# Kernel optimization log

Hardware: AMD Instinct MI355X
Metric: run time of the kernel (lower is better)

The kernel has to match this reference:

```python
import jax, jax.numpy as jnp
import numpy as np

N_THRESH = 100  # thresholds = 0.00, 0.01, ..., 0.99


def setup_inputs() -> dict:
    key = jax.random.key(0)
    k1, k2 = jax.random.split(key)
    predicted_mask = jax.random.uniform(k1, (32, 1, 1024, 1024), dtype=jnp.float32)
    gt_mask = jax.random.randint(k2, (32, 1, 1024, 1024), 0, 2, dtype=jnp.int32)
    return {"predicted_mask": predicted_mask, "gt_mask": gt_mask}


def reference(predicted_mask, gt_mask):
    # Single-pass histogram formulation of: for each t_k in arange(0,1,0.01),
    # iou_k = |(pred > t_k) & gt| / |(pred > t_k) | gt|  (torchmetrics binary Jaccard,
    # strict '>' thresholding, safe-divide -> 0 when union is empty).
    thresholds = jnp.arange(0.0, 1.0, 0.01, dtype=jnp.float32)  # [100], sorted
    pred = jnp.squeeze(predicted_mask).ravel()                  # [N] probabilities in [0,1]
    gt = jnp.squeeze(gt_mask).ravel().astype(jnp.float32)       # [N] 0/1

    # cnt[i] = number of thresholds strictly below pred[i]; pixel i satisfies
    # (pred > t_k) exactly for k in [0, cnt[i]).
    cnt = jnp.searchsorted(thresholds, pred, side='left')       # [N] int in [0, 100]

    hist_pos = jax.ops.segment_sum(gt, cnt, num_segments=N_THRESH + 1)              # [101]
    hist_all = jax.ops.segment_sum(jnp.ones_like(gt), cnt, num_segments=N_THRESH + 1)

    # TP_k = #{pred > t_k and gt==1} = sum_{c > k} hist_pos[c]  (suffix sums via cumsum)
    tp = jnp.sum(hist_pos) - jnp.cumsum(hist_pos)[:N_THRESH]        # [100]
    pred_pos = jnp.sum(hist_all) - jnp.cumsum(hist_all)[:N_THRESH]  # [100] #{pred > t_k}
    n_gt_pos = jnp.sum(gt)

    union = pred_pos + n_gt_pos - tp                                 # TP + FP + FN
    ious = jnp.where(union > 0, tp / jnp.maximum(union, 1.0), 0.0)   # safe divide -> 0
    return thresholds, ious
```

## Files before the change

### kernel.cpp

```cpp
#include <hip/hip_runtime.h>

#define N_THRESH 100
#define NBINS 101
#define NSUB 8

__global__ void zero_ws_kernel(unsigned long long* __restrict__ ws) {
    int i = threadIdx.x;
    if (i < NBINS) ws[i] = 0ull;
}

__device__ __forceinline__ int bin_of(float v) {
    int e = (int)(v * 100.0f);
    e = e < 0 ? 0 : (e > 99 ? 99 : e);
    double ed = (double)e * 0.01;
    float t0 = (float)ed;
    float t1 = (float)(ed + 0.01);
    int c = e + (t0 < v ? 1 : 0) + (t1 < v ? 1 : 0);
    return c > N_THRESH ? N_THRESH : c;
}

__device__ __forceinline__ void accum4(unsigned int* __restrict__ h,
                                       float4 p, int4 g) {
    int c0 = bin_of(p.x), c1 = bin_of(p.y), c2 = bin_of(p.z), c3 = bin_of(p.w);
    atomicAdd(&h[c0], ((unsigned int)(g.x != 0) << 16) | 1u);
    atomicAdd(&h[c1], ((unsigned int)(g.y != 0) << 16) | 1u);
    atomicAdd(&h[c2], ((unsigned int)(g.z != 0) << 16) | 1u);
    atomicAdd(&h[c3], ((unsigned int)(g.w != 0) << 16) | 1u);
}

__global__ __launch_bounds__(256) void hist_kernel(
        const float* __restrict__ pred,
        const int* __restrict__ gt,
        unsigned long long* __restrict__ ws,
        int n) {
    __shared__ unsigned int hist[NSUB][NBINS];

    const int tid = threadIdx.x;
    const int sub = ((tid >> 6) << 1) | (tid & 1);
    unsigned int* __restrict__ h = hist[sub];

    for (int i = tid; i < NSUB * NBINS; i += blockDim.x)
        (&hist[0][0])[i] = 0u;
    __syncthreads();

    const int nvec = n >> 2;
    const float4* __restrict__ p4 = (const float4*)pred;
    const int4*   __restrict__ g4 = (const int4*)gt;
    const int gsz = gridDim.x * blockDim.x;

    int i = blockIdx.x * blockDim.x + tid;
    for (; i + gsz < nvec; i += 2 * gsz) {
        float4 pa = p4[i];
        int4   ga = g4[i];
        float4 pb = p4[i + gsz];
        int4   gb = g4[i + gsz];
        accum4(h, pa, ga);
        accum4(h, pb, gb);
    }
    for (; i < nvec; i += gsz) {
        accum4(h, p4[i], g4[i]);
    }

    if (blockIdx.x == 0 && tid == 0) {
        for (int k = nvec << 2; k < n; ++k) {
            int c = bin_of(pred[k]);
            atomicAdd(&hist[0][c], ((unsigned int)(gt[k] != 0) << 16) | 1u);
        }
    }

    __syncthreads();
    if (tid < NBINS) {
        unsigned long long cnt = 0ull, pos = 0ull;
#pragma unroll
        for (int w = 0; w < NSUB; ++w) {
            unsigned int v = hist[w][tid];
            cnt += v & 0xffffu;
            pos += v >> 16;
        }
        unsigned long long s = (pos << 32) | cnt;
        if (s) atomicAdd(&ws[tid], s);
    }
}

__global__ void finalize_kernel(const unsigned long long* __restrict__ ws,
                                float* __restrict__ out) {
    __shared__ unsigned int pos[NBINS], all[NBINS];
    int k = threadIdx.x;
    if (k < NBINS) {
        unsigned long long h = ws[k];
        pos[k] = (unsigned int)(h >> 32);
        all[k] = (unsigned int)(h & 0xffffffffull);
    }
    __syncthreads();
    if (k < N_THRESH) {
        out[k] = (float)((double)k * 0.01);
        unsigned long long tp = 0, pp = 0, ngt = 0;
        for (int c = k + 1; c <= N_THRESH; ++c) { tp += pos[c]; pp += all[c]; }
        for (int c = 0; c <= N_THRESH; ++c) ngt += pos[c];
        long long uni = (long long)(pp + ngt - tp);
        double iou = (uni > 0) ? (double)tp / (double)uni : 0.0;
        out[N_THRESH + k] = (float)iou;
    }
}

extern "C" void kernel_launch(void* const* d_in, const int* in_sizes, int n_in,
                              void* d_out, int out_size, void* d_ws, size_t ws_size,
                              hipStream_t stream) {
    const float* pred = (const float*)d_in[0];
    const int*   gt   = (const int*)d_in[1];
    float* out = (float*)d_out;
    unsigned long long* ws = (unsigned long long*)d_ws;
    int n = in_sizes[0];

    zero_ws_kernel<<<1, 128, 0, stream>>>(ws);
    hist_kernel<<<2048, 256, 0, stream>>>(pred, gt, ws, n);
    finalize_kernel<<<1, 128, 0, stream>>>(ws, out);
}
```

Before: 284.2 us.

## Use bank-interleaved 32-column shared histogram and 8-way unrolled loads

Replaces the 8 sub-histograms with a transposed [bin][32] layout, so each lane's atomics go to its own LDS bank column. This is meant to cut bank conflicts and same-address atomic contention. The main loop is also unrolled to issue 8 vector loads per thread before the atomics, to raise memory-level parallelism. In exchange, shared memory grows, the final reduction reads 32 columns per bin, and register pressure rises.

Measured after the change: 282.0 us. No clear change (-0.8%).

```diff
diff --git a/kernel.cpp b/kernel.cpp
--- a/kernel.cpp
+++ b/kernel.cpp
@@ -2,7 +2,7 @@
 
 #define N_THRESH 100
 #define NBINS 101
-#define NSUB 8
+#define COLS 32
 
 __global__ void zero_ws_kernel(unsigned long long* __restrict__ ws) {
     int i = threadIdx.x;
@@ -19,27 +19,17 @@
     return c > N_THRESH ? N_THRESH : c;
 }
 
-__device__ __forceinline__ void accum4(unsigned int* __restrict__ h,
-                                       float4 p, int4 g) {
-    int c0 = bin_of(p.x), c1 = bin_of(p.y), c2 = bin_of(p.z), c3 = bin_of(p.w);
-    atomicAdd(&h[c0], ((unsigned int)(g.x != 0) << 16) | 1u);
-    atomicAdd(&h[c1], ((unsigned int)(g.y != 0) << 16) | 1u);
-    atomicAdd(&h[c2], ((unsigned int)(g.z != 0) << 16) | 1u);
-    atomicAdd(&h[c3], ((unsigned int)(g.w != 0) << 16) | 1u);
-}
-
 __global__ __launch_bounds__(256) void hist_kernel(
         const float* __restrict__ pred,
         const int* __restrict__ gt,
         unsigned long long* __restrict__ ws,
         int n) {
-    __shared__ unsigned int hist[NSUB][NBINS];
+    __shared__ unsigned int hist[NBINS][COLS];
 
     const int tid = threadIdx.x;
-    const int sub = ((tid >> 6) << 1) | (tid & 1);
-    unsigned int* __restrict__ h = hist[sub];
+    const int col = tid & (COLS - 1);
 
-    for (int i = tid; i < NSUB * NBINS; i += blockDim.x)
+    for (int i = tid; i < NBINS * COLS; i += 256)
         (&hist[0][0])[i] = 0u;
     __syncthreads();
 
@@ -49,22 +39,39 @@
     const int gsz = gridDim.x * blockDim.x;
 
     int i = blockIdx.x * blockDim.x + tid;
-    for (; i + gsz < nvec; i += 2 * gsz) {
-        float4 pa = p4[i];
-        int4   ga = g4[i];
-        float4 pb = p4[i + gsz];
-        int4   gb = g4[i + gsz];
-        accum4(h, pa, ga);
-        accum4(h, pb, gb);
+    for (; i + 7 * gsz < nvec; i += 8 * gsz) {
+        float4 p[8];
+        int4   g[8];
+#pragma unroll
+        for (int u = 0; u < 8; ++u) {
+            p[u] = p4[i + u * gsz];
+            g[u] = g4[i + u * gsz];
+        }
+#pragma unroll
+        for (int u = 0; u < 8; ++u) {
+            atomicAdd(&hist[bin_of(p[u].x)][col],
+                      1u | ((unsigned int)(g[u].x != 0) << 16));
+            atomicAdd(&hist[bin_of(p[u].y)][col],
+                      1u | ((unsigned int)(g[u].y != 0) << 16));
+            atomicAdd(&hist[bin_of(p[u].z)][col],
+                      1u | ((unsigned int)(g[u].z != 0) << 16));
+            atomicAdd(&hist[bin_of(p[u].w)][col],
+                      1u | ((unsigned int)(g[u].w != 0) << 16));
+        }
     }
     for (; i < nvec; i += gsz) {
-        accum4(h, p4[i], g4[i]);
+        float4 p = p4[i];
+        int4   g = g4[i];
+        atomicAdd(&hist[bin_of(p.x)][col], 1u | ((unsigned int)(g.x != 0) << 16));
+        atomicAdd(&hist[bin_of(p.y)][col], 1u | ((unsigned int)(g.y != 0) << 16));
+        atomicAdd(&hist[bin_of(p.z)][col], 1u | ((unsigned int)(g.z != 0) << 16));
+        atomicAdd(&hist[bin_of(p.w)][col], 1u | ((unsigned int)(g.w != 0) << 16));
     }
 
     if (blockIdx.x == 0 && tid == 0) {
         for (int k = nvec << 2; k < n; ++k) {
-            int c = bin_of(pred[k]);
-            atomicAdd(&hist[0][c], ((unsigned int)(gt[k] != 0) << 16) | 1u);
+            atomicAdd(&hist[bin_of(pred[k])][0],
+                      1u | ((unsigned int)(gt[k] != 0) << 16));
         }
     }
 
@@ -72,8 +79,8 @@
     if (tid < NBINS) {
         unsigned long long cnt = 0ull, pos = 0ull;
 #pragma unroll
-        for (int w = 0; w < NSUB; ++w) {
-            unsigned int v = hist[w][tid];
+        for (int j = 0; j < COLS; ++j) {
+            unsigned int v = hist[tid][(j + tid) & (COLS - 1)];
             cnt += v & 0xffffu;
             pos += v >> 16;
         }
```

## Stage inputs into LDS with async global_load_lds double buffering

Applied to the files above, without the earlier changes.

Replaces the direct float4/int4 global loads with tiles staged into LDS using the async global-to-LDS load builtin. A two-buffer pipeline prefetches the next step while the current one is binned with LDS atomics. Each block now works on contiguous 16K-element tiles, and a scalar path handles the ragged tail. The intent is to hide global memory latency. The cost is extra LDS traffic and a barrier per step, both competing with the LDS atomics that already dominate the histogram.

Result: slower. 296.4 us (+4.3%).

```diff
diff --git a/kernel.cpp b/kernel.cpp
--- a/kernel.cpp
+++ b/kernel.cpp
@@ -1,8 +1,15 @@
 #include <hip/hip_runtime.h>
+#include <stdint.h>
 
 #define N_THRESH 100
 #define NBINS 101
 #define NSUB 8
+#define STEP_ELEMS 2048
+#define STEPS 8
+#define TILE_ELEMS (STEP_ELEMS * STEPS)
+
+typedef __attribute__((address_space(3))) uint32_t lds_u32_t;
+typedef __attribute__((address_space(1))) uint32_t glob_u32_t;
 
 __global__ void zero_ws_kernel(unsigned long long* __restrict__ ws) {
     int i = threadIdx.x;
@@ -19,13 +26,26 @@
     return c > N_THRESH ? N_THRESH : c;
 }
 
-__device__ __forceinline__ void accum4(unsigned int* __restrict__ h,
-                                       float4 p, int4 g) {
-    int c0 = bin_of(p.x), c1 = bin_of(p.y), c2 = bin_of(p.z), c3 = bin_of(p.w);
-    atomicAdd(&h[c0], ((unsigned int)(g.x != 0) << 16) | 1u);
-    atomicAdd(&h[c1], ((unsigned int)(g.y != 0) << 16) | 1u);
-    atomicAdd(&h[c2], ((unsigned int)(g.z != 0) << 16) | 1u);
-    atomicAdd(&h[c3], ((unsigned int)(g.w != 0) << 16) | 1u);
+__device__ __forceinline__ void acc4(unsigned int* __restrict__ h,
+                                     float4 p, int4 g) {
+    atomicAdd(&h[bin_of(p.x)], 1u | ((unsigned int)(g.x != 0) << 16));
+    atomicAdd(&h[bin_of(p.y)], 1u | ((unsigned int)(g.y != 0) << 16));
+    atomicAdd(&h[bin_of(p.z)], 1u | ((unsigned int)(g.z != 0) << 16));
+    atomicAdd(&h[bin_of(p.w)], 1u | ((unsigned int)(g.w != 0) << 16));
+}
+
+__device__ __forceinline__ void stage(const float* __restrict__ pred,
+                                      const int* __restrict__ gt,
+                                      float* sp, int* sg,
+                                      int ebase, int wave, int lane) {
+    const float* srcp = pred + ebase + wave * 512 + lane * 4;
+    const int*   srcg = gt   + ebase + wave * 512 + lane * 4;
+    lds_u32_t* dp = (lds_u32_t*)(sp + wave * 512);
+    lds_u32_t* dg = (lds_u32_t*)(sg + wave * 512);
+    __builtin_amdgcn_global_load_lds((glob_u32_t*)srcp,         dp,       16, 0, 0);
+    __builtin_amdgcn_global_load_lds((glob_u32_t*)(srcp + 256), dp + 256, 16, 0, 0);
+    __builtin_amdgcn_global_load_lds((glob_u32_t*)srcg,         dg,       16, 0, 0);
+    __builtin_amdgcn_global_load_lds((glob_u32_t*)(srcg + 256), dg + 256, 16, 0, 0);
 }
 
 __global__ __launch_bounds__(256) void hist_kernel(
@@ -33,38 +53,45 @@
         const int* __restrict__ gt,
         unsigned long long* __restrict__ ws,
         int n) {
+    __shared__ __align__(16) float sp[2][STEP_ELEMS];
+    __shared__ __align__(16) int   sg[2][STEP_ELEMS];
     __shared__ unsigned int hist[NSUB][NBINS];
 
-    const int tid = threadIdx.x;
-    const int sub = ((tid >> 6) << 1) | (tid & 1);
+    const int tid  = threadIdx.x;
+    const int wave = tid >> 6;
+    const int lane = tid & 63;
+    const int sub  = (wave << 1) | (tid & 1);
     unsigned int* __restrict__ h = hist[sub];
 
-    for (int i = tid; i < NSUB * NBINS; i += blockDim.x)
+    for (int i = tid; i < NSUB * NBINS; i += 256)
         (&hist[0][0])[i] = 0u;
-    __syncthreads();
 
-    const int nvec = n >> 2;
-    const float4* __restrict__ p4 = (const float4*)pred;
-    const int4*   __restrict__ g4 = (const int4*)gt;
-    const int gsz = gridDim.x * blockDim.x;
-
-    int i = blockIdx.x * blockDim.x + tid;
-    for (; i + gsz < nvec; i += 2 * gsz) {
-        float4 pa = p4[i];
-        int4   ga = g4[i];
-        float4 pb = p4[i + gsz];
-        int4   gb = g4[i + gsz];
-        accum4(h, pa, ga);
-        accum4(h, pb, gb);
-    }
-    for (; i < nvec; i += gsz) {
-        accum4(h, p4[i], g4[i]);
-    }
-
-    if (blockIdx.x == 0 && tid == 0) {
-        for (int k = nvec << 2; k < n; ++k) {
-            int c = bin_of(pred[k]);
-            atomicAdd(&hist[0][c], ((unsigned int)(gt[k] != 0) << 16) | 1u);
+    for (long long tile = blockIdx.x; tile * TILE_ELEMS < n; tile += gridDim.x) {
+        int base = (int)(tile * TILE_ELEMS);
+        if (base + TILE_ELEMS <= n) {
+            stage(pred, gt, sp[0], sg[0], base, wave, lane);
+            __syncthreads();
+            for (int s = 0; s < STEPS; ++s) {
+                int nb = s & 1;
+                if (s + 1 < STEPS)
+                    stage(pred, gt, sp[nb ^ 1], sg[nb ^ 1],
+                          base + (s + 1) * STEP_ELEMS, wave, lane);
+                const float4* pb = (const float4*)&sp[nb][0];
+                const int4*   gb = (const int4*)&sg[nb][0];
+                float4 a  = pb[tid * 2];
+                float4 b  = pb[tid * 2 + 1];
+                int4   ga = gb[tid * 2];
+                int4   gbv = gb[tid * 2 + 1];
+                acc4(h, a, ga);
+                acc4(h, b, gbv);
+                __syncthreads();
+            }
+        } else {
+            for (int k = base + tid; k < n; k += 256) {
+                atomicAdd(&h[bin_of(pred[k])],
+                          1u | ((unsigned int)(gt[k] != 0) << 16));
+            }
+            __syncthreads();
         }
     }
 
```
